# Kernel tuning notes

Hardware: AMD Instinct MI355X
Metric: run time of the kernel (lower is better)

The kernel has to match this reference:

```python
import jax, jax.numpy as jnp
import numpy as np


def setup_inputs() -> dict:
    key = jax.random.key(0)
    k1, k2 = jax.random.split(key)
    B, N, M, D = 8, 8192, 8192, 3
    x = jax.random.normal(k1, (B, N, D), dtype=jnp.float32)
    y = jax.random.normal(k2, (B, M, D), dtype=jnp.float32)
    return {"x": x, "y": y}


def reference(x, y):
    # dist[b, i, j] = |x_bi|^2 + |y_bj|^2 - 2 * <x_bi, y_bj>
    # (same math as the torch code's rx.transpose(2,1) + ry - 2*xy, but
    #  computed with row-norm vectors instead of full NxN / MxM bmms)
    xx = jnp.sum(x * x, axis=-1)                      # [B, N]
    yy = jnp.sum(y * y, axis=-1)                      # [B, M]
    xy = jnp.einsum('bnd,bmd->bnm', x, y)             # [B, N, M]
    dist = xx[:, :, None] + yy[:, None, :] - 2.0 * xy # [B, N, M]
    dist1 = jnp.min(dist, axis=1)  # min over x points -> per-y nearest  [B, M]
    dist2 = jnp.min(dist, axis=2)  # min over y points -> per-x nearest  [B, N]
    return jnp.mean(dist1) + jnp.mean(dist2)
```

## Files before the change

### kernel.cpp

```cpp
#include <hip/hip_runtime.h>


#define B_ 8
#define N_ 8192
#define PTS (B_ * N_)
#define ROWS_TOTAL (2 * PTS)
#define NTILES 2048
#define TPB 256

typedef short bf16x8 __attribute__((ext_vector_type(8)));
typedef float f32x16 __attribute__((ext_vector_type(16)));

__device__ __forceinline__ unsigned b16(float f) {
  unsigned u = __float_as_uint(f);
  return (u + 0x7FFFu + ((u >> 16) & 1u)) >> 16;
}
__device__ __forceinline__ float bf(unsigned h) { return __uint_as_float(h << 16); }

__global__ __launch_bounds__(256) void pack_frags_k(
    const float* __restrict__ x, const float* __restrict__ y,
    uint4* __restrict__ afrag, uint4* __restrict__ bfrag) {
  const unsigned one = 0x3F80u;
  int t = blockIdx.x * 256 + threadIdx.x;
  int kind = t >> 17;
  int dir = (t >> 16) & 1;
  int p = t & 65535;
  int tile = dir * NTILES + (p >> 5), m = p & 31;
  if (kind == 0) {
    const float* src = dir ? y : x;
    const float* po = src + 3 * p;
    float v0 = po[0], v1 = po[1], v2 = po[2];
    float nv = fmaf(v0, v0, fmaf(v1, v1, v2 * v2));
    float a0 = -2.0f * v0, a1 = -2.0f * v1, a2 = -2.0f * v2;
    unsigned ah0 = b16(a0), ah1 = b16(a1), ah2 = b16(a2);
    unsigned al0 = b16(a0 - bf(ah0)), al1 = b16(a1 - bf(ah1)), al2 = b16(a2 - bf(ah2));
    unsigned nh = b16(nv), nl = b16(nv - bf(nh));
    afrag[tile * 64 + m]      = make_uint4(ah0 | (ah1 << 16), ah2 | (ah0 << 16),
                                           ah1 | (ah2 << 16), al0 | (al1 << 16));
    afrag[tile * 64 + 32 + m] = make_uint4(al2 | (nh << 16), nl | (one << 16), one, 0u);
  } else {
    const float* src = dir ? x : y;
    const float* pc = src + 3 * p;
    float c0 = pc[0], c1 = pc[1], c2 = pc[2];
    float nc = fmaf(c0, c0, fmaf(c1, c1, c2 * c2));
    unsigned yh0 = b16(c0), yh1 = b16(c1), yh2 = b16(c2);
    unsigned yl0 = b16(c0 - bf(yh0)), yl1 = b16(c1 - bf(yh1)), yl2 = b16(c2 - bf(yh2));
    unsigned nh = b16(nc), nl = b16(nc - bf(nh));
    bfrag[tile * 64 + m]      = make_uint4(yh0 | (yh1 << 16), yh2 | (yl0 << 16),
                                           yl1 | (yl2 << 16), yh0 | (yh1 << 16));
    bfrag[tile * 64 + 32 + m] = make_uint4(yh2 | (one << 16), one | (nh << 16), nl, 0u);
  }
}

__global__ __launch_bounds__(TPB, 3) void chamfer_main_k(
    const uint4* __restrict__ afrag, const uint4* __restrict__ bfrag,
    float* __restrict__ gpart) {
  int t = threadIdx.x, lane = t & 63, w = t >> 6;
  int b0 = blockIdx.x;
  int eff = ((b0 & 7) << 8) | (b0 >> 3);
  int q = eff & 3;
  int rg = eff >> 2;
  int dir = rg >> 8;
  int batch = (rg >> 5) & 7;
  int rb = rg & 31;

  int tileA0 = dir * NTILES + batch * 256 + rb * 8 + w * 2;
  bf16x8 A0 = __builtin_bit_cast(bf16x8, afrag[tileA0 * 64 + lane]);
  bf16x8 A1 = __builtin_bit_cast(bf16x8, afrag[(tileA0 + 1) * 64 + lane]);

  const uint4* bt = bfrag + (size_t)(dir * NTILES + batch * 256 + q * 64) * 64 + lane;

  f32x16 z, rm0, rm1;
#pragma unroll
  for (int r = 0; r < 16; ++r) { z[r] = 0.0f; rm0[r] = 1e30f; rm1[r] = 1e30f; }

#pragma unroll 2
  for (int j = 0; j < 64; j += 2) {
    bf16x8 B0 = __builtin_bit_cast(bf16x8, bt[(j    ) * 64]);
    bf16x8 B1 = __builtin_bit_cast(bf16x8, bt[(j + 1) * 64]);
    f32x16 acc0 = __builtin_amdgcn_mfma_f32_32x32x16_bf16(A0, B0, z, 0, 0, 0);
    f32x16 acc1 = __builtin_amdgcn_mfma_f32_32x32x16_bf16(A1, B0, z, 0, 0, 0);
    f32x16 acc2 = __builtin_amdgcn_mfma_f32_32x32x16_bf16(A0, B1, z, 0, 0, 0);
    f32x16 acc3 = __builtin_amdgcn_mfma_f32_32x32x16_bf16(A1, B1, z, 0, 0, 0);
#pragma unroll
    for (int r = 0; r < 16; ++r) {
      rm0[r] = fminf(fminf(rm0[r], acc0[r]), acc2[r]);
      rm1[r] = fminf(fminf(rm1[r], acc1[r]), acc3[r]);
    }
  }

#pragma unroll
  for (int msk = 1; msk <= 16; msk <<= 1)
#pragma unroll
    for (int r = 0; r < 16; ++r) {
      rm0[r] = fminf(rm0[r], __shfl_xor(rm0[r], msk, 64));
      rm1[r] = fminf(rm1[r], __shfl_xor(rm1[r], msk, 64));
    }

  int rowbase = dir * PTS + batch * N_ + rb * 256 + w * 64;
  float* gp = gpart + q * ROWS_TOTAL + rowbase;
  if ((lane & 31) == 0) {
    int h = lane >> 5;
#pragma unroll
    for (int r = 0; r < 16; ++r) {
      int rr = (r & 3) + 8 * (r >> 2) + 4 * h;
      gp[rr] = rm0[r];
      gp[32 + rr] = rm1[r];
    }
  }
}

__global__ __launch_bounds__(256) void chamfer_final_k(
    const float* __restrict__ gpart, float* __restrict__ out) {
  int i = blockIdx.x * 256 + threadIdx.x;
  const float4* g4 = reinterpret_cast<const float4*>(gpart);
  float4 a = g4[i];
  float4 b = g4[i + (ROWS_TOTAL / 4)];
  float4 c = g4[i + 2 * (ROWS_TOTAL / 4)];
  float4 d = g4[i + 3 * (ROWS_TOTAL / 4)];
  float s = fminf(fminf(a.x, b.x), fminf(c.x, d.x))
          + fminf(fminf(a.y, b.y), fminf(c.y, d.y))
          + fminf(fminf(a.z, b.z), fminf(c.z, d.z))
          + fminf(fminf(a.w, b.w), fminf(c.w, d.w));
  for (int off = 32; off > 0; off >>= 1) s += __shfl_down(s, off, 64);
  __shared__ float red[4];
  int lane = threadIdx.x & 63, wv = threadIdx.x >> 6;
  if (lane == 0) red[wv] = s;
  __syncthreads();
  if (threadIdx.x == 0) {
    float tt = (red[0] + red[1]) + (red[2] + red[3]);
    atomicAdd(out, tt * (1.0f / (float)PTS));
  }
}

extern "C" void kernel_launch(void* const* d_in, const int* in_sizes, int n_in,
                              void* d_out, int out_size, void* d_ws, size_t ws_size,
                              hipStream_t stream) {
  const float* x = (const float*)d_in[0];
  const float* y = (const float*)d_in[1];
  float* out = (float*)d_out;
  float* gpart = (float*)d_ws;
  uint4* afrag = (uint4*)((char*)d_ws + (size_t)4 * ROWS_TOTAL * sizeof(float));
  uint4* bfrag = afrag + (size_t)2 * NTILES * 64;

  hipMemsetAsync(out, 0, sizeof(float), stream);
  pack_frags_k<<<1024, 256, 0, stream>>>(x, y, afrag, bfrag);
  chamfer_main_k<<<2048, TPB, 0, stream>>>(afrag, bfrag, gpart);
  chamfer_final_k<<<128, 256, 0, stream>>>(gpart, out);
}
```

Before: 103.3 us.

## Stage B fragments in double-buffered LDS via async global_load_lds

The B-fragment stream is now copied into a double-buffered LDS tile with asynchronous global-to-LDS loads, in 16-tile chunks. The four waves of a block share each staged chunk instead of each wave fetching the same tiles from global memory. The next chunk is prefetched while the current one is consumed. This adds a barrier per chunk and 32KB of LDS per block, and correctness relies on the async copies completing before the barrier.

Result: no change. 104.7 us (+1.3%).

```diff
diff --git a/kernel.cpp b/kernel.cpp
--- a/kernel.cpp
+++ b/kernel.cpp
@@ -7,6 +7,7 @@
 #define ROWS_TOTAL (2 * PTS)
 #define NTILES 2048
 #define TPB 256
+#define CHUNK 16
 
 typedef short bf16x8 __attribute__((ext_vector_type(8)));
 typedef float f32x16 __attribute__((ext_vector_type(16)));
@@ -52,9 +53,24 @@
   }
 }
 
+__device__ __forceinline__ void stage_chunk(uint4* dst, const uint4* src,
+                                            int w, int lane) {
+#pragma unroll
+  for (int k = 0; k < 4; ++k) {
+    int tile = w * 4 + k;
+    const uint4* g = src + tile * 64 + lane;
+    uint4* l = dst + tile * 64;
+    __builtin_amdgcn_global_load_lds(
+        (const __attribute__((address_space(1))) unsigned int*)g,
+        (__attribute__((address_space(3))) unsigned int*)l, 16, 0, 0);
+  }
+}
+
 __global__ __launch_bounds__(TPB, 3) void chamfer_main_k(
     const uint4* __restrict__ afrag, const uint4* __restrict__ bfrag,
     float* __restrict__ gpart) {
+  __shared__ uint4 ldsB[2][CHUNK * 64];
+
   int t = threadIdx.x, lane = t & 63, w = t >> 6;
   int b0 = blockIdx.x;
   int eff = ((b0 & 7) << 8) | (b0 >> 3);
@@ -68,25 +84,35 @@
   bf16x8 A0 = __builtin_bit_cast(bf16x8, afrag[tileA0 * 64 + lane]);
   bf16x8 A1 = __builtin_bit_cast(bf16x8, afrag[(tileA0 + 1) * 64 + lane]);
 
-  const uint4* bt = bfrag + (size_t)(dir * NTILES + batch * 256 + q * 64) * 64 + lane;
+  const uint4* btile = bfrag + (size_t)(dir * NTILES + batch * 256 + q * 64) * 64;
 
   f32x16 z, rm0, rm1;
 #pragma unroll
   for (int r = 0; r < 16; ++r) { z[r] = 0.0f; rm0[r] = 1e30f; rm1[r] = 1e30f; }
 
+  stage_chunk(ldsB[0], btile, w, lane);
+  __syncthreads();
+
+  for (int ch = 0; ch < 4; ++ch) {
+    if (ch < 3)
+      stage_chunk(ldsB[(ch + 1) & 1], btile + (ch + 1) * CHUNK * 64, w, lane);
+
+    const uint4* cur = ldsB[ch & 1];
 #pragma unroll 2
-  for (int j = 0; j < 64; j += 2) {
-    bf16x8 B0 = __builtin_bit_cast(bf16x8, bt[(j    ) * 64]);
-    bf16x8 B1 = __builtin_bit_cast(bf16x8, bt[(j + 1) * 64]);
-    f32x16 acc0 = __builtin_amdgcn_mfma_f32_32x32x16_bf16(A0, B0, z, 0, 0, 0);
-    f32x16 acc1 = __builtin_amdgcn_mfma_f32_32x32x16_bf16(A1, B0, z, 0, 0, 0);
-    f32x16 acc2 = __builtin_amdgcn_mfma_f32_32x32x16_bf16(A0, B1, z, 0, 0, 0);
-    f32x16 acc3 = __builtin_amdgcn_mfma_f32_32x32x16_bf16(A1, B1, z, 0, 0, 0);
+    for (int i = 0; i < 8; ++i) {
+      bf16x8 B0 = __builtin_bit_cast(bf16x8, cur[(2 * i) * 64 + lane]);
+      bf16x8 B1 = __builtin_bit_cast(bf16x8, cur[(2 * i + 1) * 64 + lane]);
+      f32x16 acc0 = __builtin_amdgcn_mfma_f32_32x32x16_bf16(A0, B0, z, 0, 0, 0);
+      f32x16 acc1 = __builtin_amdgcn_mfma_f32_32x32x16_bf16(A1, B0, z, 0, 0, 0);
+      f32x16 acc2 = __builtin_amdgcn_mfma_f32_32x32x16_bf16(A0, B1, z, 0, 0, 0);
+      f32x16 acc3 = __builtin_amdgcn_mfma_f32_32x32x16_bf16(A1, B1, z, 0, 0, 0);
 #pragma unroll
-    for (int r = 0; r < 16; ++r) {
-      rm0[r] = fminf(fminf(rm0[r], acc0[r]), acc2[r]);
-      rm1[r] = fminf(fminf(rm1[r], acc1[r]), acc3[r]);
+      for (int r = 0; r < 16; ++r) {
+        rm0[r] = fminf(fminf(rm0[r], acc0[r]), acc2[r]);
+        rm1[r] = fminf(fminf(rm1[r], acc1[r]), acc3[r]);
+      }
     }
+    __syncthreads();
   }
 
 #pragma unroll
```

## Software-pipeline MFMA results and B-fragment loads in chamfer main loop

Applied to the files above, without the earlier changes.

Restructures the inner loop so the MFMAs for the next pair of B tiles are issued before the min-reduction of the previous iteration's accumulators. B fragments are prefetched two tiles ahead. The loop is also fully unrolled. The aim is to hide MFMA latency and global load latency behind the VALU min work. The cost is higher register pressure from keeping extra accumulator sets live, which could hurt occupancy under launch_bounds(256,3).

Result: no change. 103.0 us (-0.3%).

```diff
diff --git a/kernel.cpp b/kernel.cpp
--- a/kernel.cpp
+++ b/kernel.cpp
@@ -74,20 +74,37 @@
 #pragma unroll
   for (int r = 0; r < 16; ++r) { z[r] = 0.0f; rm0[r] = 1e30f; rm1[r] = 1e30f; }
 
-#pragma unroll 2
-  for (int j = 0; j < 64; j += 2) {
-    bf16x8 B0 = __builtin_bit_cast(bf16x8, bt[(j    ) * 64]);
-    bf16x8 B1 = __builtin_bit_cast(bf16x8, bt[(j + 1) * 64]);
-    f32x16 acc0 = __builtin_amdgcn_mfma_f32_32x32x16_bf16(A0, B0, z, 0, 0, 0);
-    f32x16 acc1 = __builtin_amdgcn_mfma_f32_32x32x16_bf16(A1, B0, z, 0, 0, 0);
-    f32x16 acc2 = __builtin_amdgcn_mfma_f32_32x32x16_bf16(A0, B1, z, 0, 0, 0);
-    f32x16 acc3 = __builtin_amdgcn_mfma_f32_32x32x16_bf16(A1, B1, z, 0, 0, 0);
+#define LD(ti) __builtin_bit_cast(bf16x8, bt[(ti) * 64])
+#define MF(Aa, Bb) __builtin_amdgcn_mfma_f32_32x32x16_bf16(Aa, Bb, z, 0, 0, 0)
+
+  bf16x8 B0v = LD(0), B1v = LD(1);
+  bf16x8 N0v = LD(2), N1v = LD(3);
+  f32x16 pP0 = MF(A0, B0v), pP1 = MF(A0, B1v);
+  f32x16 qQ0 = MF(A1, B0v), qQ1 = MF(A1, B1v);
+  B0v = N0v; B1v = N1v;
+
 #pragma unroll
-    for (int r = 0; r < 16; ++r) {
-      rm0[r] = fminf(fminf(rm0[r], acc0[r]), acc2[r]);
-      rm1[r] = fminf(fminf(rm1[r], acc1[r]), acc3[r]);
-    }
+  for (int j = 2; j < 64; j += 2) {
+    bf16x8 n0, n1;
+    if (j < 62) { n0 = LD(j + 2); n1 = LD(j + 3); }
+    f32x16 tP0 = MF(A0, B0v), tP1 = MF(A0, B1v);
+#pragma unroll
+    for (int r = 0; r < 16; ++r)
+      rm0[r] = fminf(fminf(rm0[r], pP0[r]), pP1[r]);
+    f32x16 tQ0 = MF(A1, B0v), tQ1 = MF(A1, B1v);
+#pragma unroll
+    for (int r = 0; r < 16; ++r)
+      rm1[r] = fminf(fminf(rm1[r], qQ0[r]), qQ1[r]);
+    pP0 = tP0; pP1 = tP1; qQ0 = tQ0; qQ1 = tQ1;
+    if (j < 62) { B0v = n0; B1v = n1; }
   }
+#pragma unroll
+  for (int r = 0; r < 16; ++r) {
+    rm0[r] = fminf(fminf(rm0[r], pP0[r]), pP1[r]);
+    rm1[r] = fminf(fminf(rm1[r], qQ0[r]), qQ1[r]);
+  }
+#undef LD
+#undef MF
 
 #pragma unroll
   for (int msk = 1; msk <= 16; msk <<= 1)
```

## Compute both chamfer directions from one distance matrix pass

Applied to the files above, without the earlier changes.

Previously each direction (x→y and y→x) ran a full MFMA distance sweep, so the NxM matrix was computed twice. The main kernel now computes it once and takes both row minima and column minima. Column minima go through per-wave shared memory and then to a global buffer of partials that the final kernel reduces across row blocks. This halves the MFMA work and the grid size, at the cost of extra per-iteration column reductions, cross-lane shuffles, shared-memory stores, and a larger final reduction.

New measurement: 113.8 us. 1.1x slower.

```diff
diff --git a/kernel.cpp b/kernel.cpp
--- a/kernel.cpp
+++ b/kernel.cpp
@@ -4,7 +4,6 @@
 #define B_ 8
 #define N_ 8192
 #define PTS (B_ * N_)
-#define ROWS_TOTAL (2 * PTS)
 #define NTILES 2048
 #define TPB 256
 
@@ -22,13 +21,11 @@
     uint4* __restrict__ afrag, uint4* __restrict__ bfrag) {
   const unsigned one = 0x3F80u;
   int t = blockIdx.x * 256 + threadIdx.x;
-  int kind = t >> 17;
-  int dir = (t >> 16) & 1;
+  int kind = t >> 16;
   int p = t & 65535;
-  int tile = dir * NTILES + (p >> 5), m = p & 31;
+  int tile = p >> 5, m = p & 31;
   if (kind == 0) {
-    const float* src = dir ? y : x;
-    const float* po = src + 3 * p;
+    const float* po = x + 3 * p;
     float v0 = po[0], v1 = po[1], v2 = po[2];
     float nv = fmaf(v0, v0, fmaf(v1, v1, v2 * v2));
     float a0 = -2.0f * v0, a1 = -2.0f * v1, a2 = -2.0f * v2;
@@ -39,8 +36,7 @@
                                            ah1 | (ah2 << 16), al0 | (al1 << 16));
     afrag[tile * 64 + 32 + m] = make_uint4(al2 | (nh << 16), nl | (one << 16), one, 0u);
   } else {
-    const float* src = dir ? x : y;
-    const float* pc = src + 3 * p;
+    const float* pc = y + 3 * p;
     float c0 = pc[0], c1 = pc[1], c2 = pc[2];
     float nc = fmaf(c0, c0, fmaf(c1, c1, c2 * c2));
     unsigned yh0 = b16(c0), yh1 = b16(c1), yh2 = b16(c2);
@@ -54,40 +50,55 @@
 
 __global__ __launch_bounds__(TPB, 3) void chamfer_main_k(
     const uint4* __restrict__ afrag, const uint4* __restrict__ bfrag,
-    float* __restrict__ gpart) {
+    float* __restrict__ grow, float* __restrict__ gcol) {
+  __shared__ float cmw[4][2048];
+
   int t = threadIdx.x, lane = t & 63, w = t >> 6;
   int b0 = blockIdx.x;
-  int eff = ((b0 & 7) << 8) | (b0 >> 3);
+  int eff = ((b0 & 7) << 7) | (b0 >> 3);
   int q = eff & 3;
   int rg = eff >> 2;
-  int dir = rg >> 8;
-  int batch = (rg >> 5) & 7;
+  int batch = rg >> 5;
   int rb = rg & 31;
 
-  int tileA0 = dir * NTILES + batch * 256 + rb * 8 + w * 2;
+  int tileA0 = batch * 256 + rb * 8 + w * 2;
   bf16x8 A0 = __builtin_bit_cast(bf16x8, afrag[tileA0 * 64 + lane]);
   bf16x8 A1 = __builtin_bit_cast(bf16x8, afrag[(tileA0 + 1) * 64 + lane]);
 
-  const uint4* bt = bfrag + (size_t)(dir * NTILES + batch * 256 + q * 64) * 64 + lane;
+  const uint4* bt = bfrag + (size_t)(batch * 256 + q * 64) * 64 + lane;
 
   f32x16 z, rm0, rm1;
 #pragma unroll
   for (int r = 0; r < 16; ++r) { z[r] = 0.0f; rm0[r] = 1e30f; rm1[r] = 1e30f; }
 
+#define LD(ti) __builtin_bit_cast(bf16x8, bt[(ti) * 64])
+#define MF(Aa, Bb) __builtin_amdgcn_mfma_f32_32x32x16_bf16(Aa, Bb, z, 0, 0, 0)
+
 #pragma unroll 2
   for (int j = 0; j < 64; j += 2) {
-    bf16x8 B0 = __builtin_bit_cast(bf16x8, bt[(j    ) * 64]);
-    bf16x8 B1 = __builtin_bit_cast(bf16x8, bt[(j + 1) * 64]);
-    f32x16 acc0 = __builtin_amdgcn_mfma_f32_32x32x16_bf16(A0, B0, z, 0, 0, 0);
-    f32x16 acc1 = __builtin_amdgcn_mfma_f32_32x32x16_bf16(A1, B0, z, 0, 0, 0);
-    f32x16 acc2 = __builtin_amdgcn_mfma_f32_32x32x16_bf16(A0, B1, z, 0, 0, 0);
-    f32x16 acc3 = __builtin_amdgcn_mfma_f32_32x32x16_bf16(A1, B1, z, 0, 0, 0);
+    bf16x8 B0 = LD(j), B1 = LD(j + 1);
+    f32x16 a00 = MF(A0, B0), a10 = MF(A1, B0);
+    f32x16 a01 = MF(A0, B1), a11 = MF(A1, B1);
 #pragma unroll
     for (int r = 0; r < 16; ++r) {
-      rm0[r] = fminf(fminf(rm0[r], acc0[r]), acc2[r]);
-      rm1[r] = fminf(fminf(rm1[r], acc1[r]), acc3[r]);
+      rm0[r] = fminf(fminf(rm0[r], a00[r]), a01[r]);
+      rm1[r] = fminf(fminf(rm1[r], a10[r]), a11[r]);
+    }
+    float c0 = 1e30f, c1 = 1e30f;
+#pragma unroll
+    for (int r = 0; r < 16; ++r) {
+      c0 = fminf(fminf(c0, a00[r]), a10[r]);
+      c1 = fminf(fminf(c1, a01[r]), a11[r]);
+    }
+    c0 = fminf(c0, __shfl_xor(c0, 32, 64));
+    c1 = fminf(c1, __shfl_xor(c1, 32, 64));
+    if (lane < 32) {
+      cmw[w][j * 32 + lane] = c0;
+      cmw[w][(j + 1) * 32 + lane] = c1;
     }
   }
+#undef LD
+#undef MF
 
 #pragma unroll
   for (int msk = 1; msk <= 16; msk <<= 1)
@@ -97,8 +108,8 @@
       rm1[r] = fminf(rm1[r], __shfl_xor(rm1[r], msk, 64));
     }
 
-  int rowbase = dir * PTS + batch * N_ + rb * 256 + w * 64;
-  float* gp = gpart + q * ROWS_TOTAL + rowbase;
+  int rowbase = batch * N_ + rb * 256 + w * 64;
+  float* gp = grow + (size_t)q * PTS + rowbase;
   if ((lane & 31) == 0) {
     int h = lane >> 5;
 #pragma unroll
@@ -108,24 +119,41 @@
       gp[32 + rr] = rm1[r];
     }
   }
+
+  __syncthreads();
+  float* gc = gcol + (size_t)(batch * 32 + rb) * N_ + q * 2048;
+#pragma unroll
+  for (int k = 0; k < 8; ++k) {
+    int c = k * 256 + t;
+    gc[c] = fminf(fminf(cmw[0][c], cmw[1][c]), fminf(cmw[2][c], cmw[3][c]));
+  }
 }
 
 __global__ __launch_bounds__(256) void chamfer_final_k(
-    const float* __restrict__ gpart, float* __restrict__ out) {
-  int i = blockIdx.x * 256 + threadIdx.x;
-  const float4* g4 = reinterpret_cast<const float4*>(gpart);
-  float4 a = g4[i];
-  float4 b = g4[i + (ROWS_TOTAL / 4)];
-  float4 c = g4[i + 2 * (ROWS_TOTAL / 4)];
-  float4 d = g4[i + 3 * (ROWS_TOTAL / 4)];
-  float s = fminf(fminf(a.x, b.x), fminf(c.x, d.x))
-          + fminf(fminf(a.y, b.y), fminf(c.y, d.y))
-          + fminf(fminf(a.z, b.z), fminf(c.z, d.z))
-          + fminf(fminf(a.w, b.w), fminf(c.w, d.w));
-  for (int off = 32; off > 0; off >>= 1) s += __shfl_down(s, off, 64);
+    const float* __restrict__ grow, const float* __restrict__ gcol,
+    float* __restrict__ out) {
+  int t = blockIdx.x * 256 + threadIdx.x;
+  int batch = t >> 13, c = t & 8191;
+  const float* gcb = gcol + (size_t)batch * 32 * N_ + c;
+  float cv = 1e30f;
+#pragma unroll
+  for (int s = 0; s < 32; ++s) cv = fminf(cv, gcb[(size_t)s * N_]);
+  float acc = cv;
+  if (t < (PTS / 4)) {
+    const float4* g4 = reinterpret_cast<const float4*>(grow);
+    float4 a = g4[t];
+    float4 b = g4[t + (PTS / 4)];
+    float4 c4 = g4[t + 2 * (PTS / 4)];
+    float4 d = g4[t + 3 * (PTS / 4)];
+    acc += fminf(fminf(a.x, b.x), fminf(c4.x, d.x))
+         + fminf(fminf(a.y, b.y), fminf(c4.y, d.y))
+         + fminf(fminf(a.z, b.z), fminf(c4.z, d.z))
+         + fminf(fminf(a.w, b.w), fminf(c4.w, d.w));
+  }
+  for (int off = 32; off > 0; off >>= 1) acc += __shfl_down(acc, off, 64);
   __shared__ float red[4];
   int lane = threadIdx.x & 63, wv = threadIdx.x >> 6;
-  if (lane == 0) red[wv] = s;
+  if (lane == 0) red[wv] = acc;
   __syncthreads();
   if (threadIdx.x == 0) {
     float tt = (red[0] + red[1]) + (red[2] + red[3]);
@@ -139,12 +167,13 @@
   const float* x = (const float*)d_in[0];
   const float* y = (const float*)d_in[1];
   float* out = (float*)d_out;
-  float* gpart = (float*)d_ws;
-  uint4* afrag = (uint4*)((char*)d_ws + (size_t)4 * ROWS_TOTAL * sizeof(float));
-  uint4* bfrag = afrag + (size_t)2 * NTILES * 64;
+  float* grow = (float*)d_ws;
+  float* gcol = (float*)((char*)d_ws + (size_t)4 * PTS * sizeof(float));
+  uint4* afrag = (uint4*)((char*)gcol + (size_t)32 * 8 * N_ * sizeof(float));
+  uint4* bfrag = afrag + (size_t)NTILES * 64;
 
   hipMemsetAsync(out, 0, sizeof(float), stream);
-  pack_frags_k<<<1024, 256, 0, stream>>>(x, y, afrag, bfrag);
-  chamfer_main_k<<<2048, TPB, 0, stream>>>(afrag, bfrag, gpart);
-  chamfer_final_k<<<128, 256, 0, stream>>>(gpart, out);
+  pack_frags_k<<<512, 256, 0, stream>>>(x, y, afrag, bfrag);
+  chamfer_main_k<<<1024, TPB, 0, stream>>>(afrag, bfrag, grow, gcol);
+  chamfer_final_k<<<256, 256, 0, stream>>>(grow, gcol, out);
 }
```
